# Performance work log

Hardware: AMD Instinct MI355X
Metric: run time of the kernel (lower is better)

## Reference

```python
import jax, jax.numpy as jnp
import numpy as np

B, N_Z, N_E, D = 16, 2048, 2048, 512

def setup_inputs() -> dict:
    key = jax.random.key(0)
    kz, ke, km = jax.random.split(key, 3)
    z = jax.random.normal(kz, (B, N_Z, D), dtype=jnp.float32)
    e = jax.random.normal(ke, (B, N_E, D), dtype=jnp.float32)
    M = jax.random.normal(km, (D, D), dtype=jnp.float32)  # init: normal(0, 1)
    return {"z": z, "e": e, "M": M}

def reference(z, e, M):
    # a = z @ M @ e^T : [B, Nz, Ne]
    zM = jnp.einsum('bnd,de->bne', z, M)
    a = jnp.einsum('bnd,bmd->bnm', zM, e)
    a = jax.nn.sigmoid(a)
    # softmax over dim=1 (the Nz axis), as in the torch code
    A = jax.nn.softmax(a, axis=1)
    # out = A @ e : [B, Nz, D]
    return jnp.einsum('bnm,bmd->bnd', A, e)
```

## Files before the change

### kernel.cpp

```cpp
#include <hip/hip_runtime.h>
#include <hip/hip_bf16.h>
#include <stdint.h>

#define BB 16
#define NZ 2048
#define NE 2048
#define DD 512

typedef unsigned short u16;
typedef __attribute__((ext_vector_type(8))) _Float16 f16x8;
typedef __attribute__((ext_vector_type(4))) float f32x4;

__device__ __forceinline__ u16 f2h(float f) {
  _Float16 h = (_Float16)f;
  return __builtin_bit_cast(u16, h);
}

__device__ __forceinline__ void gload_lds16(const void* g, void* l) {
  auto gp = (const __attribute__((address_space(1))) uint32_t*)g;
  auto lp = (__attribute__((address_space(3))) uint32_t*)l;
  __builtin_amdgcn_global_load_lds(gp, lp, 16, 0, 0);
}

#define FENCE() asm volatile("" ::: "memory")
#define BARRIER() do { FENCE(); __builtin_amdgcn_s_barrier(); FENCE(); } while (0)
#define WAIT_LGKM0() do { asm volatile("s_waitcnt lgkmcnt(0)" ::: "memory"); \
                          __builtin_amdgcn_sched_barrier(0); } while (0)
#define WAIT_VM(n) asm volatile("s_waitcnt vmcnt(" #n ")" ::: "memory")

__global__ void k_cvt(const float* __restrict__ in, u16* __restrict__ out, int n4) {
  int i = blockIdx.x * blockDim.x + threadIdx.x;
  int stride = gridDim.x * blockDim.x;
  for (; i < n4; i += stride) {
    float4 v = ((const float4*)in)[i];
    ushort4 o;
    o.x = f2h(v.x); o.y = f2h(v.y); o.z = f2h(v.z); o.w = f2h(v.w);
    ((ushort4*)out)[i] = o;
  }
}

__global__ void k_mt(const float* __restrict__ M, u16* __restrict__ Mt) {
  __shared__ float t[32][33];
  int bx = blockIdx.x * 32;
  int by = blockIdx.y * 32;
  for (int r = 0; r < 32; r += 8)
    t[threadIdx.y + r][threadIdx.x] = M[(size_t)(by + threadIdx.y + r) * DD + bx + threadIdx.x];
  __syncthreads();
  for (int r = 0; r < 32; r += 8)
    Mt[(size_t)(bx + threadIdx.y + r) * DD + by + threadIdx.x] = f2h(t[threadIdx.x][threadIdx.y + r]);
}

__global__ void k_et(const float* __restrict__ e, const float* __restrict__ cs,
                     u16* __restrict__ eT) {
  __shared__ float t[32][33];
  int b = blockIdx.z;
  int m0 = blockIdx.y * 32, d0 = blockIdx.x * 32;
  const float* eb = e + (size_t)b * NE * DD;
  const float* csb = cs + (size_t)b * NE;
  for (int r = 0; r < 32; r += 8) {
    int m = m0 + threadIdx.y + r;
    t[threadIdx.y + r][threadIdx.x] =
        eb[(size_t)m * DD + d0 + threadIdx.x] * (2048.0f / csb[m]);
  }
  __syncthreads();
  u16* eTb = eT + (size_t)b * DD * NE;
  for (int r = 0; r < 32; r += 8) {
    int d = d0 + threadIdx.y + r;
    eTb[(size_t)d * NE + m0 + threadIdx.x] = f2h(t[threadIdx.x][threadIdx.y + r]);
  }
}

template<int EPI, int KDIM>
__global__ __launch_bounds__(512, 2) void k_gemm(
    const u16* __restrict__ A, const u16* __restrict__ Bt, void* __restrict__ Cp,
    int Ndim, long long sAb, long long sBb, long long sCb,
    float* __restrict__ colsum, int csld)
{
  extern __shared__ char lds[];
  constexpr int NT = KDIM / 64;

  const int gx = gridDim.x, gy = gridDim.y;
  const int nwg = gx * gy * gridDim.z;
  const int hid = blockIdx.x + gx * (blockIdx.y + gy * blockIdx.z);
  const int logical = (hid & 7) * (nwg >> 3) + (hid >> 3);
  const int bx = logical % gx;
  const int rem0 = logical / gx;
  const int by = rem0 % gy;
  const int bz = rem0 / gy;

  const int tid = threadIdx.x;
  const int lane = tid & 63;
  const int wid = tid >> 6;
  const int wr = wid >> 2;
  const int wc = wid & 3;

  const int row0 = by * 256;
  const int col0 = bx * 256;

  const u16* Ab = A + (long long)bz * sAb;
  const u16* Bb = Bt + (long long)bz * sBb;

  const u16* srcA[4]; const u16* srcB[4];
#pragma unroll
  for (int c = 0; c < 4; ++c) {
    int idx = c * 512 + tid;
    int ks = idx >> 10, rm = idx & 1023;
    int mf = rm >> 6, q = (rm >> 4) & 3, p = rm & 15;
    int r = mf * 16 + p, c8 = ks * 4 + q;
    srcA[c] = Ab + (long long)(row0 + r) * KDIM + c8 * 8;
    srcB[c] = Bb + (long long)(col0 + r) * KDIM + c8 * 8;
  }

  auto stage = [&](int buf, int k0) {
#pragma unroll
    for (int c = 0; c < 4; ++c) {
      gload_lds16(srcA[c] + k0, lds + buf * 32768 + (c * 512 + wid * 64) * 16);
      gload_lds16(srcB[c] + k0, lds + 65536 + buf * 32768 + (c * 512 + wid * 64) * 16);
    }
  };

  auto ldA = [&](int buf, int ks, int m) -> f16x8 {
    return *(const f16x8*)(lds + buf * 32768 +
                           ((ks * 16 + wr * 8 + m) * 64 + lane) * 16);
  };
  auto ldB = [&](int buf, int ks, int n) -> f16x8 {
    return *(const f16x8*)(lds + 65536 + buf * 32768 +
                           ((ks * 16 + wc * 4 + n) * 64 + lane) * 16);
  };

  f32x4 acc[8][4] = {};
  f16x8 af[4], bf[4];

  stage(0, 0);
  WAIT_VM(4);
  BARRIER();

  for (int t = 0; t < NT; ++t) {
    const int buf = t & 1;
#pragma unroll
    for (int m = 0; m < 4; ++m) af[m] = ldA(buf, 0, m);
#pragma unroll
    for (int n = 0; n < 4; ++n) bf[n] = ldB(buf, 0, n);
    if (t + 1 < NT) stage(buf ^ 1, (t + 1) * 64);
    BARRIER();
    WAIT_LGKM0();
    __builtin_amdgcn_s_setprio(1);
#pragma unroll
    for (int m = 0; m < 4; ++m)
#pragma unroll
      for (int n = 0; n < 4; ++n)
        acc[m][n] = __builtin_amdgcn_mfma_f32_16x16x32_f16(af[m], bf[n], acc[m][n], 0, 0, 0);
    __builtin_amdgcn_s_setprio(0);
    BARRIER();
#pragma unroll
    for (int m = 0; m < 4; ++m) af[m] = ldA(buf, 0, 4 + m);
    BARRIER();
    WAIT_LGKM0();
    __builtin_amdgcn_s_setprio(1);
#pragma unroll
    for (int m = 0; m < 4; ++m)
#pragma unroll
      for (int n = 0; n < 4; ++n)
        acc[4 + m][n] = __builtin_amdgcn_mfma_f32_16x16x32_f16(af[m], bf[n], acc[4 + m][n], 0, 0, 0);
    __builtin_amdgcn_s_setprio(0);
    if (t + 1 < NT) { WAIT_VM(8); } else { WAIT_VM(0); }
    BARRIER();
#pragma unroll
    for (int m = 0; m < 4; ++m) af[m] = ldA(buf, 1, m);
#pragma unroll
    for (int n = 0; n < 4; ++n) bf[n] = ldB(buf, 1, n);
    BARRIER();
    WAIT_LGKM0();
    __builtin_amdgcn_s_setprio(1);
#pragma unroll
    for (int m = 0; m < 4; ++m)
#pragma unroll
      for (int n = 0; n < 4; ++n)
        acc[m][n] = __builtin_amdgcn_mfma_f32_16x16x32_f16(af[m], bf[n], acc[m][n], 0, 0, 0);
    __builtin_amdgcn_s_setprio(0);
    BARRIER();
#pragma unroll
    for (int m = 0; m < 4; ++m) af[m] = ldA(buf, 1, 4 + m);
    BARRIER();
    WAIT_LGKM0();
    __builtin_amdgcn_s_setprio(1);
#pragma unroll
    for (int m = 0; m < 4; ++m)
#pragma unroll
      for (int n = 0; n < 4; ++n)
        acc[4 + m][n] = __builtin_amdgcn_mfma_f32_16x16x32_f16(af[m], bf[n], acc[4 + m][n], 0, 0, 0);
    __builtin_amdgcn_s_setprio(0);
    if (t + 1 < NT) { WAIT_VM(4); }
    BARRIER();
  }

  const int rr = (lane >> 4) * 4;
  const int cc = lane & 15;
  if constexpr (EPI == 0) {
    u16* C = (u16*)Cp + (long long)bz * sCb;
#pragma unroll
    for (int m = 0; m < 8; ++m)
#pragma unroll
      for (int n = 0; n < 4; ++n)
#pragma unroll
        for (int j = 0; j < 4; ++j) {
          int row = row0 + wr * 128 + m * 16 + rr + j;
          int col = col0 + wc * 64 + n * 16 + cc;
          C[(long long)row * Ndim + col] = f2h(acc[m][n][j]);
        }
  } else if constexpr (EPI == 1) {
    u16* C = (u16*)Cp + (long long)bz * sCb;
    float csum[4] = {0.f, 0.f, 0.f, 0.f};
#pragma unroll
    for (int m = 0; m < 8; ++m)
#pragma unroll
      for (int n = 0; n < 4; ++n)
#pragma unroll
        for (int j = 0; j < 4; ++j) {
          float x = acc[m][n][j];
          float s = 1.f / (1.f + __expf(-x));
          float v = __expf(s);
          int row = row0 + wr * 128 + m * 16 + rr + j;
          int col = col0 + wc * 64 + n * 16 + cc;
          C[(long long)row * Ndim + col] = f2h(v);
          csum[n] += v;
        }
#pragma unroll
    for (int n = 0; n < 4; ++n) {
      float v = csum[n];
      v += __shfl_xor(v, 16, 64);
      v += __shfl_xor(v, 32, 64);
      if ((lane >> 4) == 0)
        atomicAdd(&colsum[(long long)bz * csld + col0 + wc * 64 + n * 16 + cc], v);
    }
  } else {
    float* C = (float*)Cp + (long long)bz * sCb;
#pragma unroll
    for (int m = 0; m < 8; ++m)
#pragma unroll
      for (int n = 0; n < 4; ++n)
#pragma unroll
        for (int j = 0; j < 4; ++j) {
          int row = row0 + wr * 128 + m * 16 + rr + j;
          int col = col0 + wc * 64 + n * 16 + cc;
          C[(long long)row * Ndim + col] = acc[m][n][j] * (1.0f / 2048.0f);
        }
  }
}

extern "C" void kernel_launch(void* const* d_in, const int* in_sizes, int n_in,
                              void* d_out, int out_size, void* d_ws, size_t ws_size,
                              hipStream_t stream) {
  const float* z = (const float*)d_in[0];
  const float* e = (const float*)d_in[1];
  const float* M = (const float*)d_in[2];
  float* out = (float*)d_out;
  char* ws = (char*)d_ws;

  u16* S    = (u16*)(ws + 0LL);
  u16* zM   = (u16*)(ws + 134217728LL);
  u16* zH   = (u16*)(ws + 167772160LL);
  u16* eH   = (u16*)(ws + 201326592LL);
  u16* Mt   = (u16*)(ws + 234881024LL);
  float* cs = (float*)(ws + 235405312LL);

  (void)hipFuncSetAttribute(reinterpret_cast<const void*>(&k_gemm<0, 512>),
                            hipFuncAttributeMaxDynamicSharedMemorySize, 131072);
  (void)hipFuncSetAttribute(reinterpret_cast<const void*>(&k_gemm<1, 512>),
                            hipFuncAttributeMaxDynamicSharedMemorySize, 131072);
  (void)hipFuncSetAttribute(reinterpret_cast<const void*>(&k_gemm<2, 2048>),
                            hipFuncAttributeMaxDynamicSharedMemorySize, 131072);

  hipMemsetAsync(cs, 0, (size_t)BB * NE * sizeof(float), stream);

  k_cvt<<<4096, 256, 0, stream>>>(z, zH, BB * NZ * DD / 4);
  k_cvt<<<4096, 256, 0, stream>>>(e, eH, BB * NE * DD / 4);
  k_mt<<<dim3(16, 16), dim3(32, 8), 0, stream>>>(M, Mt);

  k_gemm<0, 512><<<dim3(DD / 256, (BB * NZ) / 256, 1), 512, 131072, stream>>>(
      zH, Mt, zM, DD, 0LL, 0LL, 0LL, nullptr, 0);

  k_gemm<1, 512><<<dim3(NE / 256, NZ / 256, BB), 512, 131072, stream>>>(
      zM, eH, S, NE,
      (long long)NZ * DD, (long long)NE * DD, (long long)NZ * NE, cs, NE);

  u16* eT = zH;
  k_et<<<dim3(DD / 32, NE / 32, BB), dim3(32, 8), 0, stream>>>(e, cs, eT);

  k_gemm<2, 2048><<<dim3(DD / 256, NZ / 256, BB), 512, 131072, stream>>>(
      S, eT, out, DD,
      (long long)NZ * NE, (long long)DD * NE, (long long)NZ * DD, nullptr, 0);
}
```

Before: 326.3 us.

## Interleave A/B global-to-LDS prefetch across MFMA phases and read fp16 e in transpose

The next-tile global_load_lds prefetch is split into four pieces (A and B halves) spread across the four MFMA sub-phases instead of being issued all at once. This spreads memory traffic more evenly against compute, and the vmcnt waits are adjusted to match. The sched_barrier is removed from the LDS wait, giving the compiler more scheduling freedom. The e-transpose kernel now reads the already-converted fp16 copy of e instead of fp32, halving its read traffic at the cost of scaling from the rounded values.

Result: faster. 279.8 us (-14.3%).

```diff
diff --git a/kernel.cpp b/kernel.cpp
--- a/kernel.cpp
+++ b/kernel.cpp
@@ -16,6 +16,10 @@
   return __builtin_bit_cast(u16, h);
 }
 
+__device__ __forceinline__ float h2f(u16 h) {
+  return (float)__builtin_bit_cast(_Float16, h);
+}
+
 __device__ __forceinline__ void gload_lds16(const void* g, void* l) {
   auto gp = (const __attribute__((address_space(1))) uint32_t*)g;
   auto lp = (__attribute__((address_space(3))) uint32_t*)l;
@@ -24,8 +28,7 @@
 
 #define FENCE() asm volatile("" ::: "memory")
 #define BARRIER() do { FENCE(); __builtin_amdgcn_s_barrier(); FENCE(); } while (0)
-#define WAIT_LGKM0() do { asm volatile("s_waitcnt lgkmcnt(0)" ::: "memory"); \
-                          __builtin_amdgcn_sched_barrier(0); } while (0)
+#define WAIT_LGKM0() asm volatile("s_waitcnt lgkmcnt(0)" ::: "memory")
 #define WAIT_VM(n) asm volatile("s_waitcnt vmcnt(" #n ")" ::: "memory")
 
 __global__ void k_cvt(const float* __restrict__ in, u16* __restrict__ out, int n4) {
@@ -50,17 +53,17 @@
     Mt[(size_t)(bx + threadIdx.y + r) * DD + by + threadIdx.x] = f2h(t[threadIdx.x][threadIdx.y + r]);
 }
 
-__global__ void k_et(const float* __restrict__ e, const float* __restrict__ cs,
+__global__ void k_et(const u16* __restrict__ eH, const float* __restrict__ cs,
                      u16* __restrict__ eT) {
   __shared__ float t[32][33];
   int b = blockIdx.z;
   int m0 = blockIdx.y * 32, d0 = blockIdx.x * 32;
-  const float* eb = e + (size_t)b * NE * DD;
+  const u16* eb = eH + (size_t)b * NE * DD;
   const float* csb = cs + (size_t)b * NE;
   for (int r = 0; r < 32; r += 8) {
     int m = m0 + threadIdx.y + r;
     t[threadIdx.y + r][threadIdx.x] =
-        eb[(size_t)m * DD + d0 + threadIdx.x] * (2048.0f / csb[m]);
+        h2f(eb[(size_t)m * DD + d0 + threadIdx.x]) * (2048.0f / csb[m]);
   }
   __syncthreads();
   u16* eTb = eT + (size_t)b * DD * NE;
@@ -111,12 +114,15 @@
     srcB[c] = Bb + (long long)(col0 + r) * KDIM + c8 * 8;
   }
 
-  auto stage = [&](int buf, int k0) {
-#pragma unroll
-    for (int c = 0; c < 4; ++c) {
+  auto stageA = [&](int buf, int k0, int c0) {
+#pragma unroll
+    for (int c = c0; c < c0 + 2; ++c)
       gload_lds16(srcA[c] + k0, lds + buf * 32768 + (c * 512 + wid * 64) * 16);
+  };
+  auto stageB = [&](int buf, int k0, int c0) {
+#pragma unroll
+    for (int c = c0; c < c0 + 2; ++c)
       gload_lds16(srcB[c] + k0, lds + 65536 + buf * 32768 + (c * 512 + wid * 64) * 16);
-    }
   };
 
   auto ldA = [&](int buf, int ks, int m) -> f16x8 {
@@ -131,17 +137,20 @@
   f32x4 acc[8][4] = {};
   f16x8 af[4], bf[4];
 
-  stage(0, 0);
+  stageA(0, 0, 0); stageB(0, 0, 0);
+  stageA(0, 0, 2); stageB(0, 0, 2);
   WAIT_VM(4);
   BARRIER();
 
   for (int t = 0; t < NT; ++t) {
     const int buf = t & 1;
+    const bool pf = (t + 1 < NT);
+    const int nk0 = (t + 1) * 64;
 #pragma unroll
     for (int m = 0; m < 4; ++m) af[m] = ldA(buf, 0, m);
 #pragma unroll
     for (int n = 0; n < 4; ++n) bf[n] = ldB(buf, 0, n);
-    if (t + 1 < NT) stage(buf ^ 1, (t + 1) * 64);
+    if (pf) stageA(buf ^ 1, nk0, 0);
     BARRIER();
     WAIT_LGKM0();
     __builtin_amdgcn_s_setprio(1);
@@ -154,6 +163,7 @@
     BARRIER();
 #pragma unroll
     for (int m = 0; m < 4; ++m) af[m] = ldA(buf, 0, 4 + m);
+    if (pf) stageB(buf ^ 1, nk0, 0);
     BARRIER();
     WAIT_LGKM0();
     __builtin_amdgcn_s_setprio(1);
@@ -163,12 +173,13 @@
       for (int n = 0; n < 4; ++n)
         acc[4 + m][n] = __builtin_amdgcn_mfma_f32_16x16x32_f16(af[m], bf[n], acc[4 + m][n], 0, 0, 0);
     __builtin_amdgcn_s_setprio(0);
-    if (t + 1 < NT) { WAIT_VM(8); } else { WAIT_VM(0); }
+    if (pf) { WAIT_VM(4); } else { WAIT_VM(0); }
     BARRIER();
 #pragma unroll
     for (int m = 0; m < 4; ++m) af[m] = ldA(buf, 1, m);
 #pragma unroll
     for (int n = 0; n < 4; ++n) bf[n] = ldB(buf, 1, n);
+    if (pf) stageA(buf ^ 1, nk0, 2);
     BARRIER();
     WAIT_LGKM0();
     __builtin_amdgcn_s_setprio(1);
@@ -181,6 +192,7 @@
     BARRIER();
 #pragma unroll
     for (int m = 0; m < 4; ++m) af[m] = ldA(buf, 1, 4 + m);
+    if (pf) stageB(buf ^ 1, nk0, 2);
     BARRIER();
     WAIT_LGKM0();
     __builtin_amdgcn_s_setprio(1);
@@ -190,7 +202,7 @@
       for (int n = 0; n < 4; ++n)
         acc[4 + m][n] = __builtin_amdgcn_mfma_f32_16x16x32_f16(af[m], bf[n], acc[4 + m][n], 0, 0, 0);
     __builtin_amdgcn_s_setprio(0);
-    if (t + 1 < NT) { WAIT_VM(4); }
+    if (pf) { WAIT_VM(4); }
     BARRIER();
   }
 
@@ -285,7 +297,7 @@
       (long long)NZ * DD, (long long)NE * DD, (long long)NZ * NE, cs, NE);
 
   u16* eT = zH;
-  k_et<<<dim3(DD / 32, NE / 32, BB), dim3(32, 8), 0, stream>>>(e, cs, eT);
+  k_et<<<dim3(DD / 32, NE / 32, BB), dim3(32, 8), 0, stream>>>(eH, cs, eT);
 
   k_gemm<2, 2048><<<dim3(DD / 256, NZ / 256, BB), 512, 131072, stream>>>(
       S, eT, out, DD,
```
